# Kernel tuning notes

Hardware: AMD Instinct MI355X
Metric: run time of the kernel (lower is better)

## Reference

```python
import jax, jax.numpy as jnp
import numpy as np

B, C, H, W = 8, 256, 128, 128
M = C // 8  # query/key reduced channels (scale=8)
EPS = 1e-6


def setup_inputs() -> dict:
    key = jax.random.key(0)
    ks = jax.random.split(key, 9)
    s = 0.02
    return {
        "x": jax.random.normal(ks[0], (B, C, H, W), jnp.float32),
        "wq": jax.random.normal(ks[1], (M, C), jnp.float32) * s,
        "bq": jax.random.normal(ks[2], (M,), jnp.float32) * s,
        "wk": jax.random.normal(ks[3], (M, C), jnp.float32) * s,
        "bk": jax.random.normal(ks[4], (M,), jnp.float32) * s,
        "wv": jax.random.normal(ks[5], (C, C), jnp.float32) * s,
        "bv": jax.random.normal(ks[6], (C,), jnp.float32) * s,
        "gamma_k": jax.random.normal(ks[7], (1,), jnp.float32) * 0.1,
        "gamma_c": jax.random.normal(ks[8], (1,), jnp.float32) * 0.1,
    }


def _conv1x1(x, w, b):
    # 1x1 conv == per-pixel linear map over channels
    return jnp.einsum("oc,bchw->bohw", w, x) + b[None, :, None, None]


def reference(x, wq, bq, wk, bk, wv, bv, gamma_k, gamma_c):
    b, c, h, w = x.shape
    n = h * w

    # ---- KernelAttentionModule (softplus linear attention, O(n)) ----
    Q = jax.nn.softplus(_conv1x1(x, wq, bq)).reshape(b, -1, n).transpose(0, 2, 1)  # [b,n,m]
    K = jax.nn.softplus(_conv1x1(x, wk, bk)).reshape(b, -1, n)                      # [b,m,n]
    V = _conv1x1(x, wv, bv).reshape(b, c, n)                                        # [b,c,n]
    KV = jnp.einsum("bmn,bcn->bmc", K, V)                                           # [b,m,c]
    norm = 1.0 / jnp.einsum("bnm,bm->bn", Q, jnp.sum(K, axis=-1) + EPS)             # [b,n]
    weight_value = jnp.einsum("bnm,bmc,bn->bcn", Q, KV, norm).reshape(b, c, h, w)
    kam = x + gamma_k * weight_value

    # ---- ChannelAttentionModule (channel bmm attention) ----
    pq = x.reshape(b, c, n)
    energy = jnp.einsum("bcn,bdn->bcd", pq, pq)                                     # [b,c,c]
    energy_new = jnp.max(energy, axis=-1, keepdims=True) - energy
    attn = jax.nn.softmax(energy_new, axis=-1)
    cam = gamma_c * jnp.einsum("bcd,bdn->bcn", attn, pq).reshape(b, c, h, w)

    return kam + cam
```

## Files before the change

### kernel.cpp

```cpp
#include <hip/hip_runtime.h>
#include <math.h>

#define NPIX 16384
#define CH 256
#define MDIM 32
#define NB 8
#define EPSF 1e-6f
#define SPLIT 16
#define KCH (NPIX / SPLIT)

#define XKPART_F32OFF 16777216ull

typedef short short4v __attribute__((ext_vector_type(4)));
typedef short short8 __attribute__((ext_vector_type(8)));
typedef _Float16 half8 __attribute__((ext_vector_type(8)));
typedef float f32x4 __attribute__((ext_vector_type(4)));

__device__ inline unsigned short f2h(float v) {
    return __builtin_bit_cast(unsigned short, (_Float16)v);
}
__device__ inline float h2f(unsigned short h) {
    return (float)__builtin_bit_cast(_Float16, h);
}

__global__ void k_prep(const float* __restrict__ wq, const float* __restrict__ wk,
                       unsigned short* __restrict__ WQB, unsigned short* __restrict__ WKB)
{
    int i = blockIdx.x * 256 + threadIdx.x;
    WQB[i] = f2h(wq[i]);
    WKB[i] = f2h(wk[i]);
}

__global__ __launch_bounds__(256, 4) void k_kx(
    const float* __restrict__ x,
    const unsigned short* __restrict__ WKB, const unsigned short* __restrict__ WQB,
    const float* __restrict__ bk, const float* __restrict__ bq,
    unsigned short* __restrict__ xkpart, float* __restrict__ Ksum,
    unsigned short* __restrict__ Qg)
{
    __shared__ unsigned short xs[CH * 72];
    __shared__ unsigned short ksm[MDIM * 64];
    const int b = blockIdx.y, t = blockIdx.x, n0 = t * 64, tid = threadIdx.x;
    const int w = tid >> 6, l = tid & 63;
    const int li = l & 15, lg = l >> 4;
    const float* xb = x + (size_t)b * CH * NPIX;

    #pragma unroll
    for (int s = 0; s < 8; ++s) {
        int e8 = tid + s * 256;
        int c = e8 >> 3, j8 = e8 & 7;
        const float* src = xb + (size_t)c * NPIX + n0 + j8 * 8;
        float4 v0 = *(const float4*)src;
        float4 v1 = *(const float4*)(src + 4);
        float vv[8] = {v0.x, v0.y, v0.z, v0.w, v1.x, v1.y, v1.z, v1.w};
        short8 p;
        #pragma unroll
        for (int e = 0; e < 8; ++e) p[e] = (short)f2h(vv[e]);
        const int g = j8 ^ (c & 7) ^ ((c >> 3) & 7);
        *(short8*)&xs[c * 72 + g * 8] = p;
    }
    __syncthreads();

    {
        f32x4 accK[2], accQ[2];
        #pragma unroll
        for (int i = 0; i < 2; ++i) {
            accK[i] = (f32x4){0.f, 0.f, 0.f, 0.f};
            accQ[i] = (f32x4){0.f, 0.f, 0.f, 0.f};
        }
        const int n = w * 16 + li;
        const int gn = n >> 3, inn = n & 7;
        #pragma unroll
        for (int kc = 0; kc < 8; ++kc) {
            short8 bxw;
            #pragma unroll
            for (int e = 0; e < 8; ++e) {
                const int d = kc * 32 + lg * 8 + e;
                const int g = gn ^ e ^ ((kc * 4 + lg) & 7);
                bxw[e] = (short)xs[d * 72 + g * 8 + inn];
            }
            half8 bx = __builtin_bit_cast(half8, bxw);
            #pragma unroll
            for (int i = 0; i < 2; ++i) {
                const size_t wo = (size_t)(i * 16 + li) * CH + kc * 32 + lg * 8;
                half8 kw = __builtin_bit_cast(half8, *(const short8*)(WKB + wo));
                half8 qw = __builtin_bit_cast(half8, *(const short8*)(WQB + wo));
                accK[i] = __builtin_amdgcn_mfma_f32_16x16x32_f16(kw, bx, accK[i], 0, 0, 0);
                accQ[i] = __builtin_amdgcn_mfma_f32_16x16x32_f16(qw, bx, accQ[i], 0, 0, 0);
            }
        }
        unsigned short* qp = Qg + ((size_t)b * NPIX + n0 + n) * MDIM;
        #pragma unroll
        for (int i = 0; i < 2; ++i) {
            short4v q4;
            #pragma unroll
            for (int q = 0; q < 4; ++q) {
                const int m = i * 16 + lg * 4 + q;
                float kv = accK[i][q] + bk[m];
                kv = fmaxf(kv, 0.f) + log1pf(expf(-fabsf(kv)));
                ksm[m * 64 + (n ^ ((m & 7) << 3))] = f2h(kv);
                float qv = accQ[i][q] + bq[m];
                qv = fmaxf(qv, 0.f) + log1pf(expf(-fabsf(qv)));
                q4[q] = (short)f2h(qv);
            }
            *(short4v*)(qp + i * 16 + lg * 4) = q4;
        }
    }
    __syncthreads();

    if (tid < MDIM) {
        float s = 0.f;
        #pragma unroll
        for (int j = 0; j < 64; ++j)
            s += h2f(ksm[tid * 64 + (j ^ ((tid & 7) << 3))]);
        atomicAdd(&Ksum[b * MDIM + tid], s);
    }

    f32x4 axk[4][2];
    #pragma unroll
    for (int i = 0; i < 4; ++i)
        #pragma unroll
        for (int j = 0; j < 2; ++j) axk[i][j] = (f32x4){0.f, 0.f, 0.f, 0.f};

    #pragma unroll
    for (int ks2 = 0; ks2 < 2; ++ks2) {
        const int nc = ks2 * 32 + lg * 8;
        half8 kfr[2];
        #pragma unroll
        for (int j = 0; j < 2; ++j) {
            const int m = j * 16 + li;
            kfr[j] = __builtin_bit_cast(half8,
                *(const short8*)&ksm[m * 64 + (nc ^ ((m & 7) << 3))]);
        }
        #pragma unroll
        for (int i = 0; i < 4; ++i) {
            const int d = w * 64 + i * 16 + li;
            const int g = (nc >> 3) ^ (d & 7) ^ ((d >> 3) & 7);
            half8 xf = __builtin_bit_cast(half8, *(const short8*)&xs[d * 72 + g * 8]);
            #pragma unroll
            for (int j = 0; j < 2; ++j)
                axk[i][j] = __builtin_amdgcn_mfma_f32_16x16x32_f16(xf, kfr[j], axk[i][j], 0, 0, 0);
        }
    }

    unsigned short* xkp = xkpart + (size_t)(b * 256 + t) * MDIM * CH;
    #pragma unroll
    for (int i = 0; i < 4; ++i)
        #pragma unroll
        for (int j = 0; j < 2; ++j) {
            short4v pk;
            #pragma unroll
            for (int q = 0; q < 4; ++q) pk[q] = (short)f2h(axk[i][j][q]);
            *(short4v*)(xkp + (size_t)(j * 16 + li) * CH + w * 64 + i * 16 + lg * 4) = pk;
        }
}

__global__ void k_xkreduce(const unsigned short* __restrict__ xkpart,
                           float* __restrict__ XKR) {
    const int b = blockIdx.x >> 5, m = blockIdx.x & 31, d = threadIdx.x;
    const int t0 = blockIdx.y * 64;
    float s = 0.f;
    #pragma unroll 4
    for (int t = t0; t < t0 + 64; ++t)
        s += h2f(xkpart[(((size_t)b * 256 + t) * MDIM + m) * CH + d]);
    atomicAdd(&XKR[((size_t)b * MDIM + m) * CH + d], s);
}

__global__ void k_kv(const float* __restrict__ wv, const float* __restrict__ bv,
                     const float* __restrict__ XKR, const float* __restrict__ Ksum,
                     unsigned short* __restrict__ KVTb) {
    const int b = blockIdx.x, q = blockIdx.y;
    const int ci = threadIdx.x & 63, mg = threadIdx.x >> 6;
    const int c = q * 64 + ci;
    float s[8];
    const float bvc = bv[c];
    #pragma unroll
    for (int i = 0; i < 8; ++i) s[i] = bvc * Ksum[b * MDIM + mg * 8 + i];
    #pragma unroll 4
    for (int d = 0; d < CH; ++d) {
        float w = wv[(size_t)c * CH + d];
        #pragma unroll
        for (int i = 0; i < 8; ++i)
            s[i] = fmaf(w, XKR[((size_t)b * MDIM + mg * 8 + i) * CH + d], s[i]);
    }
    short8 p;
    #pragma unroll
    for (int i = 0; i < 8; ++i) p[i] = (short)f2h(s[i]);
    *(short8*)(KVTb + ((size_t)b * CH + c) * MDIM + mg * 8) = p;
}

__global__ __launch_bounds__(256, 4) void k_gram(const float* __restrict__ x,
                                                 float* __restrict__ enpart)
{
    __shared__ unsigned short As[128 * 72];
    __shared__ unsigned short Bs[128 * 72];

    const int tid = threadIdx.x;
    const int rt = (blockIdx.x == 2) ? 1 : 0;
    const int ct = (blockIdx.x == 0) ? 0 : 1;
    const bool diag = (rt == ct);
    const int sp = blockIdx.y, b = blockIdx.z;
    const int r0 = rt * 128, c0 = ct * 128;
    const float* xb = x + (size_t)b * CH * NPIX;
    const int k0base = sp * KCH;

    unsigned short* Bs_p = diag ? As : Bs;

    const int wave = tid >> 6, lane = tid & 63;
    const int wr = wave >> 1, wc = wave & 1;

    f32x4 acc[4][4];
    #pragma unroll
    for (int i = 0; i < 4; ++i)
        #pragma unroll
        for (int j = 0; j < 4; ++j)
            acc[i][j] = (f32x4){0.f, 0.f, 0.f, 0.f};

    const int oct = tid & 7;
    const int frow = tid >> 3;

    for (int kk = 0; kk < KCH; kk += 64) {
        __syncthreads();
        const int k0 = k0base + kk;
        #pragma unroll
        for (int half = 0; half < 2; ++half) {
            if (half && diag) continue;
            const int rowbase = half ? c0 : r0;
            unsigned short* Hs = half ? Bs : As;
            #pragma unroll
            for (int s = 0; s < 4; ++s) {
                const int r = frow + s * 32;
                const float* src = xb + (size_t)(rowbase + r) * NPIX + k0 + oct * 8;
                float4 v0 = *(const float4*)src;
                float4 v1 = *(const float4*)(src + 4);
                float vv[8] = {v0.x, v0.y, v0.z, v0.w, v1.x, v1.y, v1.z, v1.w};
                short8 p;
                #pragma unroll
                for (int e = 0; e < 8; ++e) p[e] = (short)f2h(vv[e]);
                *(short8*)&Hs[r * 72 + oct * 8] = p;
            }
        }
        __syncthreads();

        #pragma unroll
        for (int ks2 = 0; ks2 < 2; ++ks2) {
            short8 a4[4], b4[4];
            const int rbase = wr * 64 + (lane & 15);
            const int cbase = wc * 64 + (lane & 15);
            const int koff = ks2 * 32 + (lane >> 4) * 8;
            #pragma unroll
            for (int f = 0; f < 4; ++f) {
                a4[f] = *(const short8*)&As[(rbase + f * 16) * 72 + koff];
                b4[f] = *(const short8*)&Bs_p[(cbase + f * 16) * 72 + koff];
            }
            #pragma unroll
            for (int i = 0; i < 4; ++i)
                #pragma unroll
                for (int j = 0; j < 4; ++j)
                    acc[i][j] = __builtin_amdgcn_mfma_f32_16x16x32_f16(
                        __builtin_bit_cast(half8, a4[i]),
                        __builtin_bit_cast(half8, b4[j]), acc[i][j], 0, 0, 0);
        }
    }

    float* ep = enpart + (size_t)(sp * NB + b) * (CH * CH);
    const int rw = (lane >> 4) * 4;
    const int cw = lane & 15;
    #pragma unroll
    for (int i = 0; i < 4; ++i)
        #pragma unroll
        for (int j = 0; j < 4; ++j) {
            const int row = r0 + wr * 64 + i * 16 + rw;
            const int col = c0 + wc * 64 + j * 16 + cw;
            #pragma unroll
            for (int q = 0; q < 4; ++q) {
                float v = acc[i][j][q];
                ep[(size_t)(row + q) * CH + col] = v;
                if (!diag) ep[(size_t)col * CH + (row + q)] = v;
            }
        }
}

__global__ void k_softmax(const float* __restrict__ enpart,
                          const float* __restrict__ gc,
                          unsigned short* __restrict__ attnb) {
    const int b = blockIdx.x >> 8, c = blockIdx.x & 255;
    const int d = threadIdx.x;
    __shared__ float red[8];
    float e = 0.f;
    #pragma unroll
    for (int sp = 0; sp < SPLIT; ++sp)
        e += enpart[(size_t)(sp * NB + b) * (CH * CH) + (size_t)c * CH + d];
    float mn = e;
    #pragma unroll
    for (int o = 1; o < 64; o <<= 1) mn = fminf(mn, __shfl_xor(mn, o));
    if ((d & 63) == 0) red[d >> 6] = mn;
    __syncthreads();
    mn = fminf(fminf(red[0], red[1]), fminf(red[2], red[3]));
    float w = expf(mn - e);
    float s = w;
    #pragma unroll
    for (int o = 1; o < 64; o <<= 1) s += __shfl_xor(s, o);
    if ((d & 63) == 0) red[4 + (d >> 6)] = s;
    __syncthreads();
    s = red[4] + red[5] + red[6] + red[7];
    attnb[((size_t)(b * CH) + c) * CH + d] = f2h(gc[0] * w / s);
}

__global__ __launch_bounds__(256, 4) void k_final(
    const float* __restrict__ x, const unsigned short* __restrict__ Qg,
    const unsigned short* __restrict__ KVTb, const float* __restrict__ Ksum,
    const unsigned short* __restrict__ attnb, const float* __restrict__ gk,
    float* __restrict__ out)
{
    __shared__ uint2 xsTv[4096];
    unsigned char* xsT = (unsigned char*)xsTv;
    const int b = blockIdx.y, n0 = blockIdx.x * 64, tid = threadIdx.x;
    const int w = tid >> 6, l = tid & 63;
    const int li = l & 15, lg = l >> 4;
    const float* xb = x + (size_t)b * CH * NPIX;

    short8 qb[4];
    #pragma unroll
    for (int j = 0; j < 4; ++j)
        qb[j] = *(const short8*)(Qg +
            ((size_t)b * NPIX + n0 + j * 16 + li) * MDIM + lg * 8);
    float4 ks0 = *(const float4*)(Ksum + b * MDIM + lg * 8);
    float4 ks1 = *(const float4*)(Ksum + b * MDIM + lg * 8 + 4);
    const float kse[8] = {ks0.x + EPSF, ks0.y + EPSF, ks0.z + EPSF, ks0.w + EPSF,
                          ks1.x + EPSF, ks1.y + EPSF, ks1.z + EPSF, ks1.w + EPSF};

    {
        const int n4 = li * 4;
        const bool o1 = lg & 1, o2 = (lg >> 1) & 1;
        #pragma unroll 4
        for (int p = 0; p < 16; ++p) {
            const int d0 = w * 64 + p * 4;
            float4 vv = *(const float4*)(xb + (size_t)(d0 + lg) * NPIX + n0 + n4);
            float v0 = vv.x, v1 = vv.y, v2 = vv.z, v3 = vv.w;
            float r1 = __shfl_xor(o1 ? v0 : v1, 16);
            float r2 = __shfl_xor(o1 ? v2 : v3, 16);
            float a0 = o1 ? r1 : v0, a1 = o1 ? v1 : r1;
            float a2 = o1 ? r2 : v2, a3 = o1 ? v3 : r2;
            float r3 = __shfl_xor(o2 ? a0 : a2, 32);
            float r4 = __shfl_xor(o2 ? a1 : a3, 32);
            float b0 = o2 ? r3 : a0, b1 = o2 ? r4 : a1;
            float b2 = o2 ? a2 : r3, b3 = o2 ? a3 : r4;
            const int nl = n4 + lg;
            unsigned lo = (unsigned)f2h(b0) | ((unsigned)f2h(b1) << 16);
            unsigned hi = (unsigned)f2h(b2) | ((unsigned)f2h(b3) << 16);
            const int off = nl * 512 +
                ((2 * d0) ^ ((nl & 7) << 4) ^ (((nl >> 3) & 1) << 3));
            *(uint2*)(xsT + off) = make_uint2(lo, hi);
        }
    }

    f32x4 acc[4][4];
    #pragma unroll
    for (int i = 0; i < 4; ++i)
        #pragma unroll
        for (int j = 0; j < 4; ++j)
            acc[i][j] = (f32x4){0.f, 0.f, 0.f, 0.f};

    {
        const float gkv = gk[0];
        half8 qs[4];
        #pragma unroll
        for (int j = 0; j < 4; ++j) {
            float qf[8];
            float den = 0.f;
            #pragma unroll
            for (int e = 0; e < 8; ++e) {
                qf[e] = h2f((unsigned short)qb[j][e]);
                den = fmaf(qf[e], kse[e], den);
            }
            den += __shfl_xor(den, 16);
            den += __shfl_xor(den, 32);
            const float nrm = gkv / den;
            #pragma unroll
            for (int e = 0; e < 8; ++e) qs[j][e] = (_Float16)(qf[e] * nrm);
        }
        #pragma unroll
        for (int i = 0; i < 4; ++i) {
            half8 ka = __builtin_bit_cast(half8, *(const short8*)(KVTb +
                ((size_t)b * CH + w * 64 + i * 16 + li) * MDIM + lg * 8));
            #pragma unroll
            for (int j = 0; j < 4; ++j)
                acc[i][j] = __builtin_amdgcn_mfma_f32_16x16x32_f16(qs[j], ka, acc[i][j], 0, 0, 0);
        }
    }
    __syncthreads();

    const unsigned short* ab = attnb + (size_t)b * CH * CH;
    for (int kk = 0; kk < CH; kk += 32) {
        half8 bx[4];
        #pragma unroll
        for (int j = 0; j < 4; ++j) {
            const int nf = j * 16 + li;
            const int d2 = 2 * (kk + lg * 8);
            const int sw = ((nf & 7) << 4) ^ (((nf >> 3) & 1) << 3);
            uint2 h0 = *(const uint2*)(xsT + nf * 512 + (d2 ^ sw));
            uint2 h1 = *(const uint2*)(xsT + nf * 512 + ((d2 + 8) ^ sw));
            int4 tmp = make_int4(h0.x, h0.y, h1.x, h1.y);
            bx[j] = __builtin_bit_cast(half8, tmp);
        }
        #pragma unroll
        for (int i = 0; i < 4; ++i) {
            half8 af = __builtin_bit_cast(half8, *(const short8*)(ab +
                (size_t)(w * 64 + i * 16 + li) * CH + kk + lg * 8));
            #pragma unroll
            for (int j = 0; j < 4; ++j)
                acc[i][j] = __builtin_amdgcn_mfma_f32_16x16x32_f16(bx[j], af, acc[i][j], 0, 0, 0);
        }
    }

    float* outb = out + (size_t)b * CH * NPIX;
    #pragma unroll
    for (int i = 0; i < 4; ++i) {
        const int c = w * 64 + i * 16 + li;
        #pragma unroll
        for (int j = 0; j < 4; ++j) {
            const size_t idx = (size_t)c * NPIX + n0 + j * 16 + lg * 4;
            float4 xv = *(const float4*)(xb + idx);
            float4 v = make_float4(xv.x + acc[i][j][0], xv.y + acc[i][j][1],
                                   xv.z + acc[i][j][2], xv.w + acc[i][j][3]);
            *(float4*)(outb + idx) = v;
        }
    }
}

extern "C" void kernel_launch(void* const* d_in, const int* in_sizes, int n_in,
                              void* d_out, int out_size, void* d_ws, size_t ws_size,
                              hipStream_t stream)
{
    const float* x  = (const float*)d_in[0];
    const float* wq = (const float*)d_in[1];
    const float* bq = (const float*)d_in[2];
    const float* wk = (const float*)d_in[3];
    const float* bk = (const float*)d_in[4];
    const float* wv = (const float*)d_in[5];
    const float* bv = (const float*)d_in[6];
    const float* gk = (const float*)d_in[7];
    const float* gc = (const float*)d_in[8];
    float* out = (float*)d_out;
    char* wsb = (char*)d_ws;

    unsigned short* ATTB = (unsigned short*)(wsb);
    unsigned short* KVTB = (unsigned short*)(wsb + 1048576);
    float* KSUM = (float*)(wsb + 1179648);
    float* XKR  = (float*)(wsb + 1180672);
    unsigned short* WQB = (unsigned short*)(wsb + 1442816);
    unsigned short* WKB = (unsigned short*)(wsb + 1459200);
    unsigned short* QG  = (unsigned short*)(wsb + 1508352);

    unsigned short* xkpart = (unsigned short*)out;
    float* enpart = out + XKPART_F32OFF;

    hipMemsetAsync(KSUM, 0, 1024 + 262144, stream);

    k_prep<<<dim3(32), dim3(256), 0, stream>>>(wq, wk, WQB, WKB);
    k_kx<<<dim3(NPIX / 64, NB), dim3(256), 0, stream>>>(x, WKB, WQB, bk, bq,
                                                        xkpart, KSUM, QG);
    k_gram<<<dim3(3, SPLIT, NB), dim3(256), 0, stream>>>(x, enpart);
    k_xkreduce<<<dim3(NB * MDIM, 4), dim3(CH), 0, stream>>>(xkpart, XKR);
    k_kv<<<dim3(NB, 4), dim3(256), 0, stream>>>(wv, bv, XKR, KSUM, KVTB);
    k_softmax<<<dim3(NB * CH), dim3(CH), 0, stream>>>(enpart, gc, ATTB);
    k_final<<<dim3(NPIX / 64, NB), dim3(256), 0, stream>>>(x, QG, KVTB, KSUM,
                                                           ATTB, gk, out);
}
```

Before: 259.4 us.

## Merge independent gram and kx kernels, and xkreduce with softmax, into combined launches

Combines the gram (energy) kernel and the key/query projection kernel into one launch whose blocks pick a role from the block index, with gram blocks ordered first. The xk reduction and the softmax kernels are merged the same way. The goal is fewer launches, less tail idle time, and having the long gram blocks start early so the many short kx blocks fill in behind them. In exchange the shared LDS buffer is sized for the larger role, which may lower occupancy for kx blocks. The branching on block index also adds some register pressure.

```diff
diff --git a/kernel.cpp b/kernel.cpp
--- a/kernel.cpp
+++ b/kernel.cpp
@@ -11,6 +11,9 @@
 
 #define XKPART_F32OFF 16777216ull
 
+#define GRAM_BLKS 384
+#define KX_BLKS   2048
+
 typedef short short4v __attribute__((ext_vector_type(4)));
 typedef short short8 __attribute__((ext_vector_type(8)));
 typedef _Float16 half8 __attribute__((ext_vector_type(8)));
@@ -31,139 +34,266 @@
     WKB[i] = f2h(wk[i]);
 }
 
-__global__ __launch_bounds__(256, 4) void k_kx(
+__global__ __launch_bounds__(256, 4) void k_work1(
     const float* __restrict__ x,
     const unsigned short* __restrict__ WKB, const unsigned short* __restrict__ WQB,
     const float* __restrict__ bk, const float* __restrict__ bq,
     unsigned short* __restrict__ xkpart, float* __restrict__ Ksum,
-    unsigned short* __restrict__ Qg)
+    unsigned short* __restrict__ Qg, float* __restrict__ enpart)
 {
-    __shared__ unsigned short xs[CH * 72];
-    __shared__ unsigned short ksm[MDIM * 64];
-    const int b = blockIdx.y, t = blockIdx.x, n0 = t * 64, tid = threadIdx.x;
-    const int w = tid >> 6, l = tid & 63;
-    const int li = l & 15, lg = l >> 4;
-    const float* xb = x + (size_t)b * CH * NPIX;
-
-    #pragma unroll
-    for (int s = 0; s < 8; ++s) {
-        int e8 = tid + s * 256;
-        int c = e8 >> 3, j8 = e8 & 7;
-        const float* src = xb + (size_t)c * NPIX + n0 + j8 * 8;
-        float4 v0 = *(const float4*)src;
-        float4 v1 = *(const float4*)(src + 4);
-        float vv[8] = {v0.x, v0.y, v0.z, v0.w, v1.x, v1.y, v1.z, v1.w};
-        short8 p;
-        #pragma unroll
-        for (int e = 0; e < 8; ++e) p[e] = (short)f2h(vv[e]);
-        const int g = j8 ^ (c & 7) ^ ((c >> 3) & 7);
-        *(short8*)&xs[c * 72 + g * 8] = p;
-    }
-    __syncthreads();
-
-    {
-        f32x4 accK[2], accQ[2];
-        #pragma unroll
-        for (int i = 0; i < 2; ++i) {
-            accK[i] = (f32x4){0.f, 0.f, 0.f, 0.f};
-            accQ[i] = (f32x4){0.f, 0.f, 0.f, 0.f};
-        }
-        const int n = w * 16 + li;
-        const int gn = n >> 3, inn = n & 7;
-        #pragma unroll
-        for (int kc = 0; kc < 8; ++kc) {
-            short8 bxw;
-            #pragma unroll
-            for (int e = 0; e < 8; ++e) {
-                const int d = kc * 32 + lg * 8 + e;
-                const int g = gn ^ e ^ ((kc * 4 + lg) & 7);
-                bxw[e] = (short)xs[d * 72 + g * 8 + inn];
-            }
-            half8 bx = __builtin_bit_cast(half8, bxw);
+    __shared__ unsigned short ldsbuf[20480];
+    const int bid = blockIdx.x;
+    const int tid = threadIdx.x;
+
+    if (bid < GRAM_BLKS) {
+        unsigned short* As = ldsbuf;
+        unsigned short* Bs = ldsbuf + 9216;
+        const int tile = bid % 3;
+        const int rest = bid / 3;
+        const int sp = rest & 15, b = rest >> 4;
+        const int rt = (tile == 2) ? 1 : 0;
+        const int ct = (tile == 0) ? 0 : 1;
+        const bool diag = (rt == ct);
+        const int r0 = rt * 128, c0 = ct * 128;
+        const float* xb = x + (size_t)b * CH * NPIX;
+        const int k0base = sp * KCH;
+
+        unsigned short* Bs_p = diag ? As : Bs;
+
+        const int wave = tid >> 6, lane = tid & 63;
+        const int wr = wave >> 1, wc = wave & 1;
+
+        f32x4 acc[4][4];
+        #pragma unroll
+        for (int i = 0; i < 4; ++i)
+            #pragma unroll
+            for (int j = 0; j < 4; ++j)
+                acc[i][j] = (f32x4){0.f, 0.f, 0.f, 0.f};
+
+        const int oct = tid & 7;
+        const int frow = tid >> 3;
+
+        for (int kk = 0; kk < KCH; kk += 64) {
+            __syncthreads();
+            const int k0 = k0base + kk;
+            #pragma unroll
+            for (int half = 0; half < 2; ++half) {
+                if (half && diag) continue;
+                const int rowbase = half ? c0 : r0;
+                unsigned short* Hs = half ? Bs : As;
+                #pragma unroll
+                for (int s = 0; s < 4; ++s) {
+                    const int r = frow + s * 32;
+                    const float* src = xb + (size_t)(rowbase + r) * NPIX + k0 + oct * 8;
+                    float4 v0 = *(const float4*)src;
+                    float4 v1 = *(const float4*)(src + 4);
+                    float vv[8] = {v0.x, v0.y, v0.z, v0.w, v1.x, v1.y, v1.z, v1.w};
+                    short8 p;
+                    #pragma unroll
+                    for (int e = 0; e < 8; ++e) p[e] = (short)f2h(vv[e]);
+                    *(short8*)&Hs[r * 72 + oct * 8] = p;
+                }
+            }
+            __syncthreads();
+
+            #pragma unroll
+            for (int ks2 = 0; ks2 < 2; ++ks2) {
+                short8 a4[4], b4[4];
+                const int rbase = wr * 64 + (lane & 15);
+                const int cbase = wc * 64 + (lane & 15);
+                const int koff = ks2 * 32 + (lane >> 4) * 8;
+                #pragma unroll
+                for (int f = 0; f < 4; ++f) {
+                    a4[f] = *(const short8*)&As[(rbase + f * 16) * 72 + koff];
+                    b4[f] = *(const short8*)&Bs_p[(cbase + f * 16) * 72 + koff];
+                }
+                #pragma unroll
+                for (int i = 0; i < 4; ++i)
+                    #pragma unroll
+                    for (int j = 0; j < 4; ++j)
+                        acc[i][j] = __builtin_amdgcn_mfma_f32_16x16x32_f16(
+                            __builtin_bit_cast(half8, a4[i]),
+                            __builtin_bit_cast(half8, b4[j]), acc[i][j], 0, 0, 0);
+            }
+        }
+
+        float* ep = enpart + (size_t)(sp * NB + b) * (CH * CH);
+        const int rw = (lane >> 4) * 4;
+        const int cw = lane & 15;
+        #pragma unroll
+        for (int i = 0; i < 4; ++i)
+            #pragma unroll
+            for (int j = 0; j < 4; ++j) {
+                const int row = r0 + wr * 64 + i * 16 + rw;
+                const int col = c0 + wc * 64 + j * 16 + cw;
+                #pragma unroll
+                for (int q = 0; q < 4; ++q) {
+                    float v = acc[i][j][q];
+                    ep[(size_t)(row + q) * CH + col] = v;
+                    if (!diag) ep[(size_t)col * CH + (row + q)] = v;
+                }
+            }
+    } else {
+        unsigned short* xs  = ldsbuf;
+        unsigned short* ksm = ldsbuf + 18432;
+        const int u = bid - GRAM_BLKS;
+        const int b = u >> 8, t = u & 255;
+        const int n0 = t * 64;
+        const int w = tid >> 6, l = tid & 63;
+        const int li = l & 15, lg = l >> 4;
+        const float* xb = x + (size_t)b * CH * NPIX;
+
+        #pragma unroll
+        for (int s = 0; s < 8; ++s) {
+            int e8 = tid + s * 256;
+            int c = e8 >> 3, j8 = e8 & 7;
+            const float* src = xb + (size_t)c * NPIX + n0 + j8 * 8;
+            float4 v0 = *(const float4*)src;
+            float4 v1 = *(const float4*)(src + 4);
+            float vv[8] = {v0.x, v0.y, v0.z, v0.w, v1.x, v1.y, v1.z, v1.w};
+            short8 p;
+            #pragma unroll
+            for (int e = 0; e < 8; ++e) p[e] = (short)f2h(vv[e]);
+            const int g = j8 ^ (c & 7) ^ ((c >> 3) & 7);
+            *(short8*)&xs[c * 72 + g * 8] = p;
+        }
+        __syncthreads();
+
+        {
+            f32x4 accK[2], accQ[2];
             #pragma unroll
             for (int i = 0; i < 2; ++i) {
-                const size_t wo = (size_t)(i * 16 + li) * CH + kc * 32 + lg * 8;
-                half8 kw = __builtin_bit_cast(half8, *(const short8*)(WKB + wo));
-                half8 qw = __builtin_bit_cast(half8, *(const short8*)(WQB + wo));
-                accK[i] = __builtin_amdgcn_mfma_f32_16x16x32_f16(kw, bx, accK[i], 0, 0, 0);
-                accQ[i] = __builtin_amdgcn_mfma_f32_16x16x32_f16(qw, bx, accQ[i], 0, 0, 0);
-            }
-        }
-        unsigned short* qp = Qg + ((size_t)b * NPIX + n0 + n) * MDIM;
-        #pragma unroll
-        for (int i = 0; i < 2; ++i) {
-            short4v q4;
-            #pragma unroll
-            for (int q = 0; q < 4; ++q) {
-                const int m = i * 16 + lg * 4 + q;
-                float kv = accK[i][q] + bk[m];
-                kv = fmaxf(kv, 0.f) + log1pf(expf(-fabsf(kv)));
-                ksm[m * 64 + (n ^ ((m & 7) << 3))] = f2h(kv);
-                float qv = accQ[i][q] + bq[m];
-                qv = fmaxf(qv, 0.f) + log1pf(expf(-fabsf(qv)));
-                q4[q] = (short)f2h(qv);
-            }
-            *(short4v*)(qp + i * 16 + lg * 4) = q4;
-        }
-    }
-    __syncthreads();
-
-    if (tid < MDIM) {
+                accK[i] = (f32x4){0.f, 0.f, 0.f, 0.f};
+                accQ[i] = (f32x4){0.f, 0.f, 0.f, 0.f};
+            }
+            const int n = w * 16 + li;
+            const int gn = n >> 3, inn = n & 7;
+            #pragma unroll
+            for (int kc = 0; kc < 8; ++kc) {
+                short8 bxw;
+                #pragma unroll
+                for (int e = 0; e < 8; ++e) {
+                    const int d = kc * 32 + lg * 8 + e;
+                    const int g = gn ^ e ^ ((kc * 4 + lg) & 7);
+                    bxw[e] = (short)xs[d * 72 + g * 8 + inn];
+                }
+                half8 bx = __builtin_bit_cast(half8, bxw);
+                #pragma unroll
+                for (int i = 0; i < 2; ++i) {
+                    const size_t wo = (size_t)(i * 16 + li) * CH + kc * 32 + lg * 8;
+                    half8 kw = __builtin_bit_cast(half8, *(const short8*)(WKB + wo));
+                    half8 qw = __builtin_bit_cast(half8, *(const short8*)(WQB + wo));
+                    accK[i] = __builtin_amdgcn_mfma_f32_16x16x32_f16(kw, bx, accK[i], 0, 0, 0);
+                    accQ[i] = __builtin_amdgcn_mfma_f32_16x16x32_f16(qw, bx, accQ[i], 0, 0, 0);
+                }
+            }
+            unsigned short* qp = Qg + ((size_t)b * NPIX + n0 + n) * MDIM;
+            #pragma unroll
+            for (int i = 0; i < 2; ++i) {
+                short4v q4;
+                #pragma unroll
+                for (int q = 0; q < 4; ++q) {
+                    const int m = i * 16 + lg * 4 + q;
+                    float kv = accK[i][q] + bk[m];
+                    kv = fmaxf(kv, 0.f) + log1pf(expf(-fabsf(kv)));
+                    ksm[m * 64 + (n ^ ((m & 7) << 3))] = f2h(kv);
+                    float qv = accQ[i][q] + bq[m];
+                    qv = fmaxf(qv, 0.f) + log1pf(expf(-fabsf(qv)));
+                    q4[q] = (short)f2h(qv);
+                }
+                *(short4v*)(qp + i * 16 + lg * 4) = q4;
+            }
+        }
+        __syncthreads();
+
+        if (tid < MDIM) {
+            float s = 0.f;
+            #pragma unroll
+            for (int j = 0; j < 64; ++j)
+                s += h2f(ksm[tid * 64 + (j ^ ((tid & 7) << 3))]);
+            atomicAdd(&Ksum[b * MDIM + tid], s);
+        }
+
+        f32x4 axk[4][2];
+        #pragma unroll
+        for (int i = 0; i < 4; ++i)
+            #pragma unroll
+            for (int j = 0; j < 2; ++j) axk[i][j] = (f32x4){0.f, 0.f, 0.f, 0.f};
+
+        #pragma unroll
+        for (int ks2 = 0; ks2 < 2; ++ks2) {
+            const int nc = ks2 * 32 + lg * 8;
+            half8 kfr[2];
+            #pragma unroll
+            for (int j = 0; j < 2; ++j) {
+                const int m = j * 16 + li;
+                kfr[j] = __builtin_bit_cast(half8,
+                    *(const short8*)&ksm[m * 64 + (nc ^ ((m & 7) << 3))]);
+            }
+            #pragma unroll
+            for (int i = 0; i < 4; ++i) {
+                const int d = w * 64 + i * 16 + li;
+                const int g = (nc >> 3) ^ (d & 7) ^ ((d >> 3) & 7);
+                half8 xf = __builtin_bit_cast(half8, *(const short8*)&xs[d * 72 + g * 8]);
+                #pragma unroll
+                for (int j = 0; j < 2; ++j)
+                    axk[i][j] = __builtin_amdgcn_mfma_f32_16x16x32_f16(xf, kfr[j], axk[i][j], 0, 0, 0);
+            }
+        }
+
+        unsigned short* xkp = xkpart + (size_t)(b * 256 + t) * MDIM * CH;
+        #pragma unroll
+        for (int i = 0; i < 4; ++i)
+            #pragma unroll
+            for (int j = 0; j < 2; ++j) {
+                short4v pk;
+                #pragma unroll
+                for (int q = 0; q < 4; ++q) pk[q] = (short)f2h(axk[i][j][q]);
+                *(short4v*)(xkp + (size_t)(j * 16 + li) * CH + w * 64 + i * 16 + lg * 4) = pk;
+            }
+    }
+}
+
+__global__ void k_work2(const unsigned short* __restrict__ xkpart,
+                        float* __restrict__ XKR,
+                        const float* __restrict__ enpart,
+                        const float* __restrict__ gc,
+                        unsigned short* __restrict__ attnb)
+{
+    __shared__ float red[8];
+    const int bid = blockIdx.x;
+    if (bid < 1024) {
+        const int bx = bid & 255;
+        const int b = bx >> 5, m = bx & 31, d = threadIdx.x;
+        const int t0 = (bid >> 8) * 64;
         float s = 0.f;
-        #pragma unroll
-        for (int j = 0; j < 64; ++j)
-            s += h2f(ksm[tid * 64 + (j ^ ((tid & 7) << 3))]);
-        atomicAdd(&Ksum[b * MDIM + tid], s);
-    }
-
-    f32x4 axk[4][2];
-    #pragma unroll
-    for (int i = 0; i < 4; ++i)
-        #pragma unroll
-        for (int j = 0; j < 2; ++j) axk[i][j] = (f32x4){0.f, 0.f, 0.f, 0.f};
-
-    #pragma unroll
-    for (int ks2 = 0; ks2 < 2; ++ks2) {
-        const int nc = ks2 * 32 + lg * 8;
-        half8 kfr[2];
-        #pragma unroll
-        for (int j = 0; j < 2; ++j) {
-            const int m = j * 16 + li;
-            kfr[j] = __builtin_bit_cast(half8,
-                *(const short8*)&ksm[m * 64 + (nc ^ ((m & 7) << 3))]);
-        }
-        #pragma unroll
-        for (int i = 0; i < 4; ++i) {
-            const int d = w * 64 + i * 16 + li;
-            const int g = (nc >> 3) ^ (d & 7) ^ ((d >> 3) & 7);
-            half8 xf = __builtin_bit_cast(half8, *(const short8*)&xs[d * 72 + g * 8]);
-            #pragma unroll
-            for (int j = 0; j < 2; ++j)
-                axk[i][j] = __builtin_amdgcn_mfma_f32_16x16x32_f16(xf, kfr[j], axk[i][j], 0, 0, 0);
-        }
-    }
-
-    unsigned short* xkp = xkpart + (size_t)(b * 256 + t) * MDIM * CH;
-    #pragma unroll
-    for (int i = 0; i < 4; ++i)
-        #pragma unroll
-        for (int j = 0; j < 2; ++j) {
-            short4v pk;
-            #pragma unroll
-            for (int q = 0; q < 4; ++q) pk[q] = (short)f2h(axk[i][j][q]);
-            *(short4v*)(xkp + (size_t)(j * 16 + li) * CH + w * 64 + i * 16 + lg * 4) = pk;
-        }
-}
-
-__global__ void k_xkreduce(const unsigned short* __restrict__ xkpart,
-                           float* __restrict__ XKR) {
-    const int b = blockIdx.x >> 5, m = blockIdx.x & 31, d = threadIdx.x;
-    const int t0 = blockIdx.y * 64;
-    float s = 0.f;
-    #pragma unroll 4
-    for (int t = t0; t < t0 + 64; ++t)
-        s += h2f(xkpart[(((size_t)b * 256 + t) * MDIM + m) * CH + d]);
-    atomicAdd(&XKR[((size_t)b * MDIM + m) * CH + d], s);
+        #pragma unroll 4
+        for (int t = t0; t < t0 + 64; ++t)
+            s += h2f(xkpart[(((size_t)b * 256 + t) * MDIM + m) * CH + d]);
+        atomicAdd(&XKR[((size_t)b * MDIM + m) * CH + d], s);
+    } else {
+        const int bid2 = bid - 1024;
+        const int b = bid2 >> 8, c = bid2 & 255;
+        const int d = threadIdx.x;
+        float e = 0.f;
+        #pragma unroll
+        for (int sp = 0; sp < SPLIT; ++sp)
+            e += enpart[(size_t)(sp * NB + b) * (CH * CH) + (size_t)c * CH + d];
+        float mn = e;
+        #pragma unroll
+        for (int o = 1; o < 64; o <<= 1) mn = fminf(mn, __shfl_xor(mn, o));
+        if ((d & 63) == 0) red[d >> 6] = mn;
+        __syncthreads();
+        mn = fminf(fminf(red[0], red[1]), fminf(red[2], red[3]));
+        float w = expf(mn - e);
+        float s = w;
+        #pragma unroll
+        for (int o = 1; o < 64; o <<= 1) s += __shfl_xor(s, o);
+        if ((d & 63) == 0) red[4 + (d >> 6)] = s;
+        __syncthreads();
+        s = red[4] + red[5] + red[6] + red[7];
+        attnb[((size_t)(b * CH) + c) * CH + d] = f2h(gc[0] * w / s);
+    }
 }
 
 __global__ void k_kv(const float* __restrict__ wv, const float* __restrict__ bv,
@@ -187,124 +317,6 @@
     #pragma unroll
     for (int i = 0; i < 8; ++i) p[i] = (short)f2h(s[i]);
     *(short8*)(KVTb + ((size_t)b * CH + c) * MDIM + mg * 8) = p;
-}
-
-__global__ __launch_bounds__(256, 4) void k_gram(const float* __restrict__ x,
-                                                 float* __restrict__ enpart)
-{
-    __shared__ unsigned short As[128 * 72];
-    __shared__ unsigned short Bs[128 * 72];
-
-    const int tid = threadIdx.x;
-    const int rt = (blockIdx.x == 2) ? 1 : 0;
-    const int ct = (blockIdx.x == 0) ? 0 : 1;
-    const bool diag = (rt == ct);
-    const int sp = blockIdx.y, b = blockIdx.z;
-    const int r0 = rt * 128, c0 = ct * 128;
-    const float* xb = x + (size_t)b * CH * NPIX;
-    const int k0base = sp * KCH;
-
-    unsigned short* Bs_p = diag ? As : Bs;
-
-    const int wave = tid >> 6, lane = tid & 63;
-    const int wr = wave >> 1, wc = wave & 1;
-
-    f32x4 acc[4][4];
-    #pragma unroll
-    for (int i = 0; i < 4; ++i)
-        #pragma unroll
-        for (int j = 0; j < 4; ++j)
-            acc[i][j] = (f32x4){0.f, 0.f, 0.f, 0.f};
-
-    const int oct = tid & 7;
-    const int frow = tid >> 3;
-
-    for (int kk = 0; kk < KCH; kk += 64) {
-        __syncthreads();
-        const int k0 = k0base + kk;
-        #pragma unroll
-        for (int half = 0; half < 2; ++half) {
-            if (half && diag) continue;
-            const int rowbase = half ? c0 : r0;
-            unsigned short* Hs = half ? Bs : As;
-            #pragma unroll
-            for (int s = 0; s < 4; ++s) {
-                const int r = frow + s * 32;
-                const float* src = xb + (size_t)(rowbase + r) * NPIX + k0 + oct * 8;
-                float4 v0 = *(const float4*)src;
-                float4 v1 = *(const float4*)(src + 4);
-                float vv[8] = {v0.x, v0.y, v0.z, v0.w, v1.x, v1.y, v1.z, v1.w};
-                short8 p;
-                #pragma unroll
-                for (int e = 0; e < 8; ++e) p[e] = (short)f2h(vv[e]);
-                *(short8*)&Hs[r * 72 + oct * 8] = p;
-            }
-        }
-        __syncthreads();
-
-        #pragma unroll
-        for (int ks2 = 0; ks2 < 2; ++ks2) {
-            short8 a4[4], b4[4];
-            const int rbase = wr * 64 + (lane & 15);
-            const int cbase = wc * 64 + (lane & 15);
-            const int koff = ks2 * 32 + (lane >> 4) * 8;
-            #pragma unroll
-            for (int f = 0; f < 4; ++f) {
-                a4[f] = *(const short8*)&As[(rbase + f * 16) * 72 + koff];
-                b4[f] = *(const short8*)&Bs_p[(cbase + f * 16) * 72 + koff];
-            }
-            #pragma unroll
-            for (int i = 0; i < 4; ++i)
-                #pragma unroll
-                for (int j = 0; j < 4; ++j)
-                    acc[i][j] = __builtin_amdgcn_mfma_f32_16x16x32_f16(
-                        __builtin_bit_cast(half8, a4[i]),
-                        __builtin_bit_cast(half8, b4[j]), acc[i][j], 0, 0, 0);
-        }
-    }
-
-    float* ep = enpart + (size_t)(sp * NB + b) * (CH * CH);
-    const int rw = (lane >> 4) * 4;
-    const int cw = lane & 15;
-    #pragma unroll
-    for (int i = 0; i < 4; ++i)
-        #pragma unroll
-        for (int j = 0; j < 4; ++j) {
-            const int row = r0 + wr * 64 + i * 16 + rw;
-            const int col = c0 + wc * 64 + j * 16 + cw;
-            #pragma unroll
-            for (int q = 0; q < 4; ++q) {
-                float v = acc[i][j][q];
-                ep[(size_t)(row + q) * CH + col] = v;
-                if (!diag) ep[(size_t)col * CH + (row + q)] = v;
-            }
-        }
-}
-
-__global__ void k_softmax(const float* __restrict__ enpart,
-                          const float* __restrict__ gc,
-                          unsigned short* __restrict__ attnb) {
-    const int b = blockIdx.x >> 8, c = blockIdx.x & 255;
-    const int d = threadIdx.x;
-    __shared__ float red[8];
-    float e = 0.f;
-    #pragma unroll
-    for (int sp = 0; sp < SPLIT; ++sp)
-        e += enpart[(size_t)(sp * NB + b) * (CH * CH) + (size_t)c * CH + d];
-    float mn = e;
-    #pragma unroll
-    for (int o = 1; o < 64; o <<= 1) mn = fminf(mn, __shfl_xor(mn, o));
-    if ((d & 63) == 0) red[d >> 6] = mn;
-    __syncthreads();
-    mn = fminf(fminf(red[0], red[1]), fminf(red[2], red[3]));
-    float w = expf(mn - e);
-    float s = w;
-    #pragma unroll
-    for (int o = 1; o < 64; o <<= 1) s += __shfl_xor(s, o);
-    if ((d & 63) == 0) red[4 + (d >> 6)] = s;
-    __syncthreads();
-    s = red[4] + red[5] + red[6] + red[7];
-    attnb[((size_t)(b * CH) + c) * CH + d] = f2h(gc[0] * w / s);
 }
 
 __global__ __launch_bounds__(256, 4) void k_final(
@@ -459,12 +471,10 @@
     hipMemsetAsync(KSUM, 0, 1024 + 262144, stream);
 
     k_prep<<<dim3(32), dim3(256), 0, stream>>>(wq, wk, WQB, WKB);
-    k_kx<<<dim3(NPIX / 64, NB), dim3(256), 0, stream>>>(x, WKB, WQB, bk, bq,
-                                                        xkpart, KSUM, QG);
-    k_gram<<<dim3(3, SPLIT, NB), dim3(256), 0, stream>>>(x, enpart);
-    k_xkreduce<<<dim3(NB * MDIM, 4), dim3(CH), 0, stream>>>(xkpart, XKR);
+    k_work1<<<dim3(GRAM_BLKS + KX_BLKS), dim3(256), 0, stream>>>(
+        x, WKB, WQB, bk, bq, xkpart, KSUM, QG, enpart);
+    k_work2<<<dim3(3072), dim3(256), 0, stream>>>(xkpart, XKR, enpart, gc, ATTB);
     k_kv<<<dim3(NB, 4), dim3(256), 0, stream>>>(wv, bv, XKR, KSUM, KVTB);
-    k_softmax<<<dim3(NB * CH), dim3(CH), 0, stream>>>(enpart, gc, ATTB);
     k_final<<<dim3(NPIX / 64, NB), dim3(256), 0, stream>>>(x, QG, KVTB, KSUM,
                                                            ATTB, gk, out);
 }
```

After: 227.5 us. 1.14x faster.
